# Optimization experiments

Measured on AMD Instinct MI355X. Metric: run time of the kernel, lower is better.

The kernel has to match this reference:

```python
import jax, jax.numpy as jnp
import numpy as np

D = 1024; NH = 16; HD = D // NH; B = 2; L = 2048
BASE_FAST = (1.0 + 5.0 ** 0.5) / 2.0
BASE_SLOW = 1618.0
BASE_GLU = 16180.0
ALPHA_ATTN = 0.42; ALPHA_MLP = 1.07; ALPHA_ADV = 1.0
H_GATE = max(8, D // 4)   # rope_gate hidden
H_NU = max(4, D // 8)     # DuplexViscosity hidden
LN_EPS = 1e-5


def _rope_cos_sin(seq_len, dim, base, dtype=jnp.float32):
    idx = jnp.arange(0, dim, 2, dtype=dtype) / float(dim)
    inv = 1.0 / (base ** idx)
    t = jnp.arange(seq_len, dtype=dtype)
    freqs = jnp.outer(t, inv)                       # (L, D/2)
    emb = jnp.concatenate([freqs, freqs], axis=-1)  # (L, D)
    return jnp.cos(emb)[None], jnp.sin(emb)[None]   # (1, L, D)


def _rotate_half(x):
    x1, x2 = jnp.split(x, 2, axis=-1)
    return jnp.concatenate([-x2, x1], axis=-1)


def _apply_rope(x, cos, sin):
    return x * cos + _rotate_half(x) * sin


def setup_inputs() -> dict:
    key = jax.random.key(0)
    ks = jax.random.split(key, 16)
    std = 0.02
    # all Linear weights stored as (in, out) so forward is x @ W + b
    return {
        "z": jax.random.normal(ks[0], (B, L, D), jnp.float32),
        "Wq": jax.random.normal(ks[1], (D, D), jnp.float32) * std,
        "bq": jnp.zeros((D,), jnp.float32),
        "Wk": jax.random.normal(ks[2], (D, D), jnp.float32) * std,
        "bk": jnp.zeros((D,), jnp.float32),
        "Wv": jax.random.normal(ks[3], (D, D), jnp.float32) * std,
        "bv": jnp.zeros((D,), jnp.float32),
        "Wcoh": jax.random.normal(ks[4], (D, D), jnp.float32) * std,
        "gamma": jnp.zeros((1,), jnp.float32),
        "rg_w1": jax.random.normal(ks[5], (D, H_GATE), jnp.float32) * std,
        "rg_b1": jnp.zeros((H_GATE,), jnp.float32),
        "rg_w2": jax.random.normal(ks[6], (H_GATE, 1), jnp.float32) * std,
        "rg_b2": jnp.zeros((1,), jnp.float32),
        "nu_diff": jnp.asarray(0.2, jnp.float32),
        "nu_adv": jnp.asarray(0.01, jnp.float32),
        "nu_w1": jax.random.normal(ks[7], (D, H_NU), jnp.float32) * std,
        "nu_b1": jnp.zeros((H_NU,), jnp.float32),
        "nu_w2": jax.random.normal(ks[8], (H_NU, 1), jnp.float32) * std,
        "nu_b2": jnp.zeros((1,), jnp.float32),
        "Wu": jax.random.normal(ks[9], (D, D), jnp.float32) * std,
        "bu": jnp.zeros((D,), jnp.float32),
        "Wg": jax.random.normal(ks[10], (D, D), jnp.float32) * std,
        "bg": jnp.zeros((D,), jnp.float32),
        "ln_w": jnp.ones((D,), jnp.float32),
        "ln_b": jnp.zeros((D,), jnp.float32),
        "Cw": jax.random.normal(ks[11], (D, D), jnp.float32) * std,
        "Cb": jnp.zeros((D,), jnp.float32),
    }


def reference(z, Wq, bq, Wk, bk, Wv, bv, Wcoh, gamma, rg_w1, rg_b1, rg_w2, rg_b2,
              nu_diff, nu_adv, nu_w1, nu_b1, nu_w2, nu_b2, Wu, bu, Wg, bg,
              ln_w, ln_b, Cw, Cb):
    b, l, d = z.shape
    dt = z.dtype
    # causal cumulative mean pool[t] = mean(z[0..t])
    pool = jnp.cumsum(z, axis=1) / jnp.arange(1, l + 1, dtype=dt)[None, :, None]

    # QKV projections
    Q = z @ Wq + bq
    K_raw = z @ Wk + bk
    V = z @ Wv + bv

    # global coherence bias: (B, Lq, Lk)
    gk = pool @ Wcoh
    gb = jnp.einsum('bld,bmd->blm', gk, K_raw) * (d ** -0.5)
    gb = jnp.tanh(gamma[0]) * gb

    # hybrid RoPE gate (small MLP on pool, exact gelu as in torch)
    gate = jax.nn.sigmoid(jax.nn.gelu(pool @ rg_w1 + rg_b1, approximate=False) @ rg_w2 + rg_b2)  # (B,L,1)
    cos_f, sin_f = _rope_cos_sin(l, d, BASE_FAST, dt)
    cos_s, sin_s = _rope_cos_sin(l, d, BASE_SLOW, dt)
    cos = gate * cos_f + (1.0 - gate) * cos_s
    sin = gate * sin_f + (1.0 - gate) * sin_s
    Qr = _apply_rope(Q, cos, sin)
    Kr = _apply_rope(K_raw, cos, sin)

    # multi-head causal attention with fused coherence bias
    Qh = Qr.reshape(b, l, NH, HD).transpose(0, 2, 1, 3)
    Kh = Kr.reshape(b, l, NH, HD).transpose(0, 2, 1, 3)
    Vh = V.reshape(b, l, NH, HD).transpose(0, 2, 1, 3)
    logits = jnp.einsum('bhld,bhmd->bhlm', Qh, Kh) * (HD ** -0.5)
    logits = logits + gb[:, None]
    causal = jnp.tril(jnp.ones((l, l), bool))
    logits = jnp.where(causal[None, None], logits, -jnp.inf)
    attn = jax.nn.softmax(logits, axis=-1)
    attn_out = jnp.einsum('bhlm,bhmd->bhld', attn, Vh).transpose(0, 2, 1, 3).reshape(b, l, d)
    attn_w = attn.mean(axis=1)

    # DuplexViscosity on causal pool
    delta = jnp.tanh(jnp.tanh(pool @ nu_w1 + nu_b1) @ nu_w2 + nu_b2) * jnp.abs(nu_adv)
    nu_b = jnp.abs(nu_diff) + delta  # (B,L,1)

    # GLU branch with fixed slow-base RoPE
    cos_g, sin_g = _rope_cos_sin(l, d, BASE_GLU, dt)
    z_glu = _apply_rope(z, cos_g, sin_g)
    bilinear = (z_glu @ Wu + bu) * (z_glu @ Wg + bg)
    adv = -(ALPHA_ADV * nu_b) * bilinear
    mu = adv.mean(axis=-1, keepdims=True)
    var = ((adv - mu) ** 2).mean(axis=-1, keepdims=True)
    adv_n = (adv - mu) * jax.lax.rsqrt(var + LN_EPS) * ln_w + ln_b
    mlp_out = adv_n @ Cw + Cb

    z_next = z + ALPHA_ATTN * attn_out + ALPHA_MLP * mlp_out
    return z_next, attn_w
```

## Files before the change

kernel.cpp:

```cpp
#include <hip/hip_runtime.h>

#define DD 1024
#define NHH 16
#define HDD 64
#define BB 2
#define LL 2048
#define MM (BB*LL)
#define HG 256
#define HN 128

#define LOG_FAST 0.48121182f
#define LOG_SLOW 7.3889461f
#define LOG_GLU  9.6915312f
#define SCL 0.18033688f

typedef __attribute__((ext_vector_type(8))) short short8;
typedef __attribute__((ext_vector_type(4))) float f32x4;

__device__ __forceinline__ float gelu_f(float x) {
    return 0.5f * x * (1.0f + erff(x * 0.70710678f));
}

__device__ __forceinline__ ushort f2b(float x) {
    unsigned u = __float_as_uint(x);
    unsigned r = (u + 0x7FFFu + ((u >> 16) & 1u)) >> 16;
    return (ushort)r;
}

__device__ __forceinline__ float b2f(ushort x) {
    return __uint_as_float(((unsigned)x) << 16);
}

__device__ __forceinline__ void gl_lds16(const ushort* g, ushort* l) {
    __builtin_amdgcn_global_load_lds(
        (const __attribute__((address_space(1))) unsigned int*)g,
        (__attribute__((address_space(3))) unsigned int*)l, 16, 0, 0);
}

#define SWZC(row, c8) (((((row) << 3) | ((c8) ^ ((row) & 7)))) << 3)

__device__ __forceinline__ void stage_tile(const ushort* gsrc, int rstride,
                                           ushort* lds, int tid) {
    int wid = tid >> 6;
#pragma unroll
    for (int r = 0; r < 2; ++r) {
        int c = r * 256 + tid;
        int row = c >> 3;
        int c8 = (c & 7) ^ (row & 7);
        gl_lds16(gsrc + (size_t)row * rstride + c8 * 8,
                 lds + (size_t)(r * 256 + wid * 64) * 8);
    }
}

#define LCH 128
#define NCH 16
__global__ void pool_scan1(const float* __restrict__ z, float* __restrict__ pool,
                           float* __restrict__ ctot) {
    int ch = blockIdx.x, dg = blockIdx.y, b = blockIdx.z;
    int d = dg * 256 + threadIdx.x;
    const float* zp = z + ((size_t)b * LL + ch * LCH) * DD + d;
    float* pp = pool + ((size_t)b * LL + ch * LCH) * DD + d;
    float s = 0.f;
    for (int t = 0; t < LCH; ++t) {
        s += zp[(size_t)t * DD];
        pp[(size_t)t * DD] = s;
    }
    ctot[((size_t)b * NCH + ch) * DD + d] = s;
}
__global__ void pool_scan2(const float* __restrict__ ctot, float* __restrict__ pool) {
    int ch = blockIdx.x, dg = blockIdx.y, b = blockIdx.z;
    int d = dg * 256 + threadIdx.x;
    float off = 0.f;
    for (int c = 0; c < ch; ++c) off += ctot[((size_t)b * NCH + c) * DD + d];
    int t0 = ch * LCH;
    float* pp = pool + ((size_t)b * LL + t0) * DD + d;
    for (int t = 0; t < LCH; ++t) {
        pp[(size_t)t * DD] = (pp[(size_t)t * DD] + off) / (float)(t0 + t + 1);
    }
}

__global__ void f2b_kernel(const float* __restrict__ in, ushort* __restrict__ out) {
    size_t i = ((size_t)blockIdx.x * 256 + threadIdx.x) * 4;
    float4 v = *(const float4*)&in[i];
    ushort4 o;
    o.x = f2b(v.x); o.y = f2b(v.y); o.z = f2b(v.z); o.w = f2b(v.w);
    *(ushort4*)&out[i] = o;
}

__global__ void f2bT_kernel(const float* __restrict__ W, ushort* __restrict__ Wt, int Ndim) {
    __shared__ float t[32][33];
    int n0 = blockIdx.x * 32, k0 = blockIdx.y * 32;
    int tx = threadIdx.x & 31, ty = threadIdx.x >> 5;
#pragma unroll
    for (int j = 0; j < 4; ++j)
        t[ty + j * 8][tx] = W[(size_t)(k0 + ty + j * 8) * Ndim + n0 + tx];
    __syncthreads();
#pragma unroll
    for (int j = 0; j < 4; ++j)
        Wt[(size_t)(n0 + ty + j * 8) * 1024 + k0 + tx] = f2b(t[tx][ty + j * 8]);
}

__global__ void f2bT3_kernel(const float* __restrict__ W0, const float* __restrict__ W1,
                             const float* __restrict__ W2, ushort* __restrict__ Wt) {
    const float* W = blockIdx.z == 0 ? W0 : (blockIdx.z == 1 ? W1 : W2);
    ushort* dst = Wt + (size_t)blockIdx.z * 1024 * 1024;
    __shared__ float t[32][33];
    int n0 = blockIdx.x * 32, k0 = blockIdx.y * 32;
    int tx = threadIdx.x & 31, ty = threadIdx.x >> 5;
#pragma unroll
    for (int j = 0; j < 4; ++j)
        t[ty + j * 8][tx] = W[(size_t)(k0 + ty + j * 8) * 1024 + n0 + tx];
    __syncthreads();
#pragma unroll
    for (int j = 0; j < 4; ++j)
        dst[(size_t)(n0 + ty + j * 8) * 1024 + k0 + tx] = f2b(t[tx][ty + j * 8]);
}

__global__ __launch_bounds__(256) void gemm_mfma(
        const ushort* __restrict__ A, const ushort* __restrict__ Wt,
        const float* __restrict__ bias, float* __restrict__ C, int Ndim) {
    __shared__ ushort As[4096];
    __shared__ ushort Bs[4096];
    int tid = threadIdx.x;
    int wid = tid >> 6, lane = tid & 63;
    int n0 = blockIdx.x * 128, m0 = blockIdx.y * 128;
    int wm = wid >> 1, wn = wid & 1;
    int quad = lane >> 4, l16 = lane & 15;

    f32x4 acc[4][4];
#pragma unroll
    for (int mi = 0; mi < 4; ++mi)
#pragma unroll
        for (int ni = 0; ni < 4; ++ni) acc[mi][ni] = (f32x4){0.f, 0.f, 0.f, 0.f};

    int c0 = wid * 128 + lane;
    int c1 = c0 + 64;
    const ushort* Ag0 = A + (size_t)(m0 + (c0 & 127)) * 1024 + (c0 >> 7) * 8;
    const ushort* Ag1 = A + (size_t)(m0 + (c1 & 127)) * 1024 + (c1 >> 7) * 8;
    const ushort* Bg0 = Wt + (size_t)(n0 + (c0 & 127)) * 1024 + (c0 >> 7) * 8;
    const ushort* Bg1 = Wt + (size_t)(n0 + (c1 & 127)) * 1024 + (c1 >> 7) * 8;
    ushort* Al0 = As + wid * 1024;
    ushort* Al1 = As + wid * 1024 + 512;
    ushort* Bl0 = Bs + wid * 1024;
    ushort* Bl1 = Bs + wid * 1024 + 512;

    const ushort* a_rd = &As[(quad * 128 + wm * 64 + l16) * 8];
    const ushort* b_rd = &Bs[(quad * 128 + wn * 64 + l16) * 8];

    for (int kb = 0; kb < 1024; kb += 32) {
        gl_lds16(Ag0 + kb, Al0);
        gl_lds16(Ag1 + kb, Al1);
        gl_lds16(Bg0 + kb, Bl0);
        gl_lds16(Bg1 + kb, Bl1);
        __syncthreads();
        short8 af[4], bf[4];
#pragma unroll
        for (int mi = 0; mi < 4; ++mi)
            af[mi] = *(const short8*)(a_rd + mi * 16 * 8);
#pragma unroll
        for (int ni = 0; ni < 4; ++ni)
            bf[ni] = *(const short8*)(b_rd + ni * 16 * 8);
#pragma unroll
        for (int mi = 0; mi < 4; ++mi)
#pragma unroll
            for (int ni = 0; ni < 4; ++ni)
                acc[mi][ni] = __builtin_amdgcn_mfma_f32_16x16x32_bf16(
                    af[mi], bf[ni], acc[mi][ni], 0, 0, 0);
        __syncthreads();
    }
    int bcol[4];
    float bval[4];
#pragma unroll
    for (int ni = 0; ni < 4; ++ni) {
        bcol[ni] = n0 + wn * 64 + ni * 16 + l16;
        bval[ni] = bias ? bias[bcol[ni]] : 0.f;
    }
#pragma unroll
    for (int mi = 0; mi < 4; ++mi) {
#pragma unroll
        for (int r = 0; r < 4; ++r) {
            int row = m0 + wm * 64 + mi * 16 + quad * 4 + r;
            float* Cp = C + (size_t)row * Ndim;
#pragma unroll
            for (int ni = 0; ni < 4; ++ni)
                Cp[bcol[ni]] = acc[mi][ni][r] + bval[ni];
        }
    }
}

__global__ __launch_bounds__(256) void gemm_mfma3(
        const ushort* __restrict__ A, const ushort* __restrict__ Wt,
        const float* __restrict__ b0, const float* __restrict__ b1,
        const float* __restrict__ b2, float* __restrict__ C) {
    int zid = blockIdx.z;
    const ushort* W = Wt + (size_t)zid * 1024 * 1024;
    const float* bias = zid == 0 ? b0 : (zid == 1 ? b1 : b2);
    float* Cz = C + (size_t)zid * (size_t)MM * DD;
    __shared__ ushort As[4096];
    __shared__ ushort Bs[4096];
    int tid = threadIdx.x;
    int wid = tid >> 6, lane = tid & 63;
    int n0 = blockIdx.x * 128, m0 = blockIdx.y * 128;
    int wm = wid >> 1, wn = wid & 1;
    int quad = lane >> 4, l16 = lane & 15;

    f32x4 acc[4][4];
#pragma unroll
    for (int mi = 0; mi < 4; ++mi)
#pragma unroll
        for (int ni = 0; ni < 4; ++ni) acc[mi][ni] = (f32x4){0.f, 0.f, 0.f, 0.f};

    int c0 = wid * 128 + lane;
    int c1 = c0 + 64;
    const ushort* Ag0 = A + (size_t)(m0 + (c0 & 127)) * 1024 + (c0 >> 7) * 8;
    const ushort* Ag1 = A + (size_t)(m0 + (c1 & 127)) * 1024 + (c1 >> 7) * 8;
    const ushort* Bg0 = W + (size_t)(n0 + (c0 & 127)) * 1024 + (c0 >> 7) * 8;
    const ushort* Bg1 = W + (size_t)(n0 + (c1 & 127)) * 1024 + (c1 >> 7) * 8;
    ushort* Al0 = As + wid * 1024;
    ushort* Al1 = As + wid * 1024 + 512;
    ushort* Bl0 = Bs + wid * 1024;
    ushort* Bl1 = Bs + wid * 1024 + 512;

    const ushort* a_rd = &As[(quad * 128 + wm * 64 + l16) * 8];
    const ushort* b_rd = &Bs[(quad * 128 + wn * 64 + l16) * 8];

    for (int kb = 0; kb < 1024; kb += 32) {
        gl_lds16(Ag0 + kb, Al0);
        gl_lds16(Ag1 + kb, Al1);
        gl_lds16(Bg0 + kb, Bl0);
        gl_lds16(Bg1 + kb, Bl1);
        __syncthreads();
        short8 af[4], bf[4];
#pragma unroll
        for (int mi = 0; mi < 4; ++mi)
            af[mi] = *(const short8*)(a_rd + mi * 16 * 8);
#pragma unroll
        for (int ni = 0; ni < 4; ++ni)
            bf[ni] = *(const short8*)(b_rd + ni * 16 * 8);
#pragma unroll
        for (int mi = 0; mi < 4; ++mi)
#pragma unroll
            for (int ni = 0; ni < 4; ++ni)
                acc[mi][ni] = __builtin_amdgcn_mfma_f32_16x16x32_bf16(
                    af[mi], bf[ni], acc[mi][ni], 0, 0, 0);
        __syncthreads();
    }
    float bval[4];
    int bcol[4];
#pragma unroll
    for (int ni = 0; ni < 4; ++ni) {
        bcol[ni] = n0 + wn * 64 + ni * 16 + l16;
        bval[ni] = bias[bcol[ni]];
    }
#pragma unroll
    for (int mi = 0; mi < 4; ++mi) {
#pragma unroll
        for (int r = 0; r < 4; ++r) {
            int row = m0 + wm * 64 + mi * 16 + quad * 4 + r;
            float* Cp = Cz + (size_t)row * 1024;
#pragma unroll
            for (int ni = 0; ni < 4; ++ni)
                Cp[bcol[ni]] = acc[mi][ni][r] + bval[ni];
        }
    }
}

__global__ __launch_bounds__(256) void gemm_mfma_b16out(
        const ushort* __restrict__ A, const ushort* __restrict__ Wt,
        ushort* __restrict__ C, int Ndim) {
    __shared__ ushort As[4096];
    __shared__ ushort Bs[4096];
    int tid = threadIdx.x;
    int wid = tid >> 6, lane = tid & 63;
    int n0 = blockIdx.x * 128, m0 = blockIdx.y * 128;
    int wm = wid >> 1, wn = wid & 1;
    int quad = lane >> 4, l16 = lane & 15;

    f32x4 acc[4][4];
#pragma unroll
    for (int mi = 0; mi < 4; ++mi)
#pragma unroll
        for (int ni = 0; ni < 4; ++ni) acc[mi][ni] = (f32x4){0.f, 0.f, 0.f, 0.f};

    int c0 = wid * 128 + lane;
    int c1 = c0 + 64;
    const ushort* Ag0 = A + (size_t)(m0 + (c0 & 127)) * 1024 + (c0 >> 7) * 8;
    const ushort* Ag1 = A + (size_t)(m0 + (c1 & 127)) * 1024 + (c1 >> 7) * 8;
    const ushort* Bg0 = Wt + (size_t)(n0 + (c0 & 127)) * 1024 + (c0 >> 7) * 8;
    const ushort* Bg1 = Wt + (size_t)(n0 + (c1 & 127)) * 1024 + (c1 >> 7) * 8;
    ushort* Al0 = As + wid * 1024;
    ushort* Al1 = As + wid * 1024 + 512;
    ushort* Bl0 = Bs + wid * 1024;
    ushort* Bl1 = Bs + wid * 1024 + 512;

    const ushort* a_rd = &As[(quad * 128 + wm * 64 + l16) * 8];
    const ushort* b_rd = &Bs[(quad * 128 + wn * 64 + l16) * 8];

    for (int kb = 0; kb < 1024; kb += 32) {
        gl_lds16(Ag0 + kb, Al0);
        gl_lds16(Ag1 + kb, Al1);
        gl_lds16(Bg0 + kb, Bl0);
        gl_lds16(Bg1 + kb, Bl1);
        __syncthreads();
        short8 af[4], bf[4];
#pragma unroll
        for (int mi = 0; mi < 4; ++mi)
            af[mi] = *(const short8*)(a_rd + mi * 16 * 8);
#pragma unroll
        for (int ni = 0; ni < 4; ++ni)
            bf[ni] = *(const short8*)(b_rd + ni * 16 * 8);
#pragma unroll
        for (int mi = 0; mi < 4; ++mi)
#pragma unroll
            for (int ni = 0; ni < 4; ++ni)
                acc[mi][ni] = __builtin_amdgcn_mfma_f32_16x16x32_bf16(
                    af[mi], bf[ni], acc[mi][ni], 0, 0, 0);
        __syncthreads();
    }
#pragma unroll
    for (int mi = 0; mi < 4; ++mi) {
#pragma unroll
        for (int r = 0; r < 4; ++r) {
            int row = m0 + wm * 64 + mi * 16 + quad * 4 + r;
            ushort* Cp = C + (size_t)row * Ndim;
#pragma unroll
            for (int ni = 0; ni < 4; ++ni)
                Cp[n0 + wn * 64 + ni * 16 + l16] = f2b(acc[mi][ni][r]);
        }
    }
}

__global__ __launch_bounds__(256) void gb_mfma(
        const ushort* __restrict__ gk16, const ushort* __restrict__ K16r,
        const float* __restrict__ gamma, ushort* __restrict__ gb) {
    int lt = blockIdx.x >> 4, mt = blockIdx.x & 15;
    if (mt > lt) return;
    int b = blockIdx.y;
    __shared__ ushort As[4096];
    __shared__ ushort Bs[4096];
    int tid = threadIdx.x;
    int wid = tid >> 6, lane = tid & 63;
    int l0 = lt * 128, m0 = mt * 128;
    int wm = wid >> 1, wn = wid & 1;
    int quad = lane >> 4, l16 = lane & 15;

    f32x4 acc[4][4];
#pragma unroll
    for (int mi = 0; mi < 4; ++mi)
#pragma unroll
        for (int ni = 0; ni < 4; ++ni) acc[mi][ni] = (f32x4){0.f, 0.f, 0.f, 0.f};

    int c0 = wid * 128 + lane;
    int c1 = c0 + 64;
    const ushort* Ag0 = gk16 + ((size_t)b * LL + l0 + (c0 & 127)) * 1024 + (c0 >> 7) * 8;
    const ushort* Ag1 = gk16 + ((size_t)b * LL + l0 + (c1 & 127)) * 1024 + (c1 >> 7) * 8;
    const ushort* Bg0 = K16r + ((size_t)b * LL + m0 + (c0 & 127)) * 1024 + (c0 >> 7) * 8;
    const ushort* Bg1 = K16r + ((size_t)b * LL + m0 + (c1 & 127)) * 1024 + (c1 >> 7) * 8;
    ushort* Al0 = As + wid * 1024;
    ushort* Al1 = As + wid * 1024 + 512;
    ushort* Bl0 = Bs + wid * 1024;
    ushort* Bl1 = Bs + wid * 1024 + 512;

    const ushort* a_rd = &As[(quad * 128 + wm * 64 + l16) * 8];
    const ushort* b_rd = &Bs[(quad * 128 + wn * 64 + l16) * 8];

    for (int kb = 0; kb < 1024; kb += 32) {
        gl_lds16(Ag0 + kb, Al0);
        gl_lds16(Ag1 + kb, Al1);
        gl_lds16(Bg0 + kb, Bl0);
        gl_lds16(Bg1 + kb, Bl1);
        __syncthreads();
        short8 af[4], bf[4];
#pragma unroll
        for (int mi = 0; mi < 4; ++mi)
            af[mi] = *(const short8*)(a_rd + mi * 16 * 8);
#pragma unroll
        for (int ni = 0; ni < 4; ++ni)
            bf[ni] = *(const short8*)(b_rd + ni * 16 * 8);
#pragma unroll
        for (int mi = 0; mi < 4; ++mi)
#pragma unroll
            for (int ni = 0; ni < 4; ++ni)
                acc[mi][ni] = __builtin_amdgcn_mfma_f32_16x16x32_bf16(
                    af[mi], bf[ni], acc[mi][ni], 0, 0, 0);
        __syncthreads();
    }
    float scale = tanhf(gamma[0]) * 0.25f;
#pragma unroll
    for (int mi = 0; mi < 4; ++mi) {
#pragma unroll
        for (int r = 0; r < 4; ++r) {
            int row = l0 + wm * 64 + mi * 16 + quad * 4 + r;
            ushort* Cp = gb + ((size_t)b * LL + row) * LL;
#pragma unroll
            for (int ni = 0; ni < 4; ++ni)
                Cp[m0 + wn * 64 + ni * 16 + l16] = f2b(acc[mi][ni][r] * scale);
        }
    }
}

__global__ __launch_bounds__(256) void gate_fin_kernel(
        const float* __restrict__ H1, const float* __restrict__ w2,
        const float* __restrict__ b2, float* __restrict__ gate) {
    int row = blockIdx.x, tid = threadIdx.x;
    float x = H1[(size_t)row * HG + tid];
    float val = gelu_f(x) * w2[tid];
    for (int off = 32; off; off >>= 1) val += __shfl_down(val, off);
    __shared__ float part[4];
    if ((tid & 63) == 0) part[tid >> 6] = val;
    __syncthreads();
    if (tid == 0) {
        float acc = part[0] + part[1] + part[2] + part[3] + b2[0];
        gate[row] = 1.f / (1.f + expf(-acc));
    }
}

__global__ __launch_bounds__(128) void nu_fin_kernel(
        const float* __restrict__ N1, const float* __restrict__ w2,
        const float* __restrict__ b2, const float* __restrict__ nu_diff,
        const float* __restrict__ nu_adv, float* __restrict__ nub) {
    int row = blockIdx.x, tid = threadIdx.x;
    float t = tanhf(N1[(size_t)row * HN + tid]);
    float val = t * w2[tid];
    for (int off = 32; off; off >>= 1) val += __shfl_down(val, off);
    __shared__ float part[2];
    if ((tid & 63) == 0) part[tid >> 6] = val;
    __syncthreads();
    if (tid == 0) {
        float acc = part[0] + part[1] + b2[0];
        nub[row] = fabsf(nu_diff[0]) + tanhf(acc) * fabsf(nu_adv[0]);
    }
}

__global__ void rope_qk_bf16(const float* __restrict__ Q, const float* __restrict__ K,
                             const float* __restrict__ gate,
                             ushort* __restrict__ Q16, ushort* __restrict__ K16) {
    int idx = blockIdx.x * 256 + threadIdx.x;
    int row = idx >> 9;
    int i = idx & 511;
    int b = row >> 11, t = row & (LL - 1);
    float g = gate[row];
    float fi = (float)i * (1.0f / 512.0f);
    float tf = (float)t;
    float af = tf * expf(-fi * LOG_FAST);
    float as = tf * expf(-fi * LOG_SLOW);
    float c = g * cosf(af) + (1.f - g) * cosf(as);
    float s = g * sinf(af) + (1.f - g) * sinf(as);
    size_t base = (size_t)row * DD;
    float x = Q[base + i], y = Q[base + 512 + i];
    float q1 = x * c - y * s, q2 = y * c + x * s;
    x = K[base + i]; y = K[base + 512 + i];
    float k1 = x * c - y * s, k2 = y * c + x * s;
    int h1 = i >> 6, d1 = i & 63;
    size_t o1 = ((size_t)(b * 16 + h1) * LL + t) * 64 + d1;
    size_t o2 = ((size_t)(b * 16 + 8 + h1) * LL + t) * 64 + d1;
    Q16[o1] = f2b(q1); Q16[o2] = f2b(q2);
    K16[o1] = f2b(k1); K16[o2] = f2b(k2);
}

__global__ __launch_bounds__(256) void vt16_kernel(const float* __restrict__ V,
                                                   ushort* __restrict__ VT) {
    __shared__ ushort t[64][72];
    int lb = blockIdx.x, hb = blockIdx.y, b = blockIdx.z;
    int tid = threadIdx.x;
    {
        int l = tid >> 2, c0 = (tid & 3) * 16;
        const float* Vp = V + ((size_t)(b * LL) + lb * 64 + l) * DD + hb * 64 + c0;
#pragma unroll
        for (int j = 0; j < 4; ++j) {
            float4 v = *(const float4*)(Vp + j * 4);
            t[l][c0 + j * 4 + 0] = f2b(v.x);
            t[l][c0 + j * 4 + 1] = f2b(v.y);
            t[l][c0 + j * 4 + 2] = f2b(v.z);
            t[l][c0 + j * 4 + 3] = f2b(v.w);
        }
    }
    __syncthreads();
    {
        int d = tid >> 2, l0 = (tid & 3) * 16;
        ushort tmp[16];
#pragma unroll
        for (int j = 0; j < 16; ++j) tmp[j] = t[l0 + j][d];
        ushort* Op = VT + ((size_t)((b * 16 + hb) * 64) + d) * LL + lb * 64 + l0;
        *(ushort4*)(Op + 0)  = *(ushort4*)&tmp[0];
        *(ushort4*)(Op + 4)  = *(ushort4*)&tmp[4];
        *(ushort4*)(Op + 8)  = *(ushort4*)&tmp[8];
        *(ushort4*)(Op + 12) = *(ushort4*)&tmp[12];
    }
}

__global__ void rope_glu_b16(const float* __restrict__ z, ushort* __restrict__ zg) {
    int idx = blockIdx.x * 256 + threadIdx.x;
    int row = idx >> 9;
    int i = idx & 511;
    int t = row & (LL - 1);
    float fi = (float)i * (1.0f / 512.0f);
    float ag = (float)t * expf(-fi * LOG_GLU);
    float c = cosf(ag), s = sinf(ag);
    size_t base = (size_t)row * DD;
    float x = z[base + i], y = z[base + 512 + i];
    zg[base + i]       = f2b(x * c - y * s);
    zg[base + 512 + i] = f2b(y * c + x * s);
}

__global__ __launch_bounds__(256, 3) void attn_flash_mfma(
        const ushort* __restrict__ Q16, const ushort* __restrict__ K16,
        const ushort* __restrict__ VT16, const ushort* __restrict__ gb16,
        float* __restrict__ attn_out, float* __restrict__ stats) {
    int h = blockIdx.x, qt = 31 - blockIdx.y, b = blockIdx.z;
    __shared__ ushort Qs[4096], Ks[2][4096], Vs[2][4096];
    __shared__ ushort Ps[4][1152];
    int tid = threadIdx.x, wid = tid >> 6, lane = tid & 63;
    int quad = lane >> 4, l16 = lane & 15;
    const ushort* Qg = Q16 + ((size_t)(b * 16 + h) * LL) * 64;
    const ushort* Kg = K16 + ((size_t)(b * 16 + h) * LL) * 64;
    const ushort* Vg = VT16 + ((size_t)(b * 16 + h) * 64) * LL;
    const ushort* gbB = gb16 + (size_t)b * LL * LL;
    float* stB = stats + ((size_t)(b * 16 + h) * LL) * 2;
    int qrow = wid * 16 + quad * 4;
    int q0 = qt * 64;

    stage_tile(Qg + (size_t)q0 * 64, 64, Qs, tid);
    stage_tile(Kg, 64, Ks[0], tid);
    stage_tile(Vg, LL, Vs[0], tid);
    __syncthreads();
    short8 qf[2];
#pragma unroll
    for (int ks = 0; ks < 2; ++ks)
        qf[ks] = *(const short8*)(Qs + SWZC(wid * 16 + l16, ks * 4 + quad));

    short ov = (l16 == 0) ? (short)0x3F80 : (short)0;
    short8 onesf = {ov, ov, ov, ov, ov, ov, ov, ov};

    f32x4 ofr[5];
    float m_r[4];
#pragma unroll
    for (int nt = 0; nt < 5; ++nt) ofr[nt] = (f32x4){0.f, 0.f, 0.f, 0.f};
#pragma unroll
    for (int r = 0; r < 4; ++r) m_r[r] = -3e38f;

    for (int kt = 0; kt <= qt; ++kt) {
        int cur = kt & 1;
        int k0 = kt * 64;
        ushort gw[4][4];
#pragma unroll
        for (int r = 0; r < 4; ++r) {
            const ushort* gp = gbB + (size_t)(q0 + qrow + r) * LL + k0 + l16;
#pragma unroll
            for (int nt = 0; nt < 4; ++nt) gw[nt][r] = gp[nt * 16];
        }
        if (kt < qt) {
            stage_tile(Kg + (size_t)(k0 + 64) * 64, 64, Ks[cur ^ 1], tid);
            stage_tile(Vg + (k0 + 64), LL, Vs[cur ^ 1], tid);
        }
        f32x4 sf[4];
#pragma unroll
        for (int nt = 0; nt < 4; ++nt)
#pragma unroll
            for (int r = 0; r < 4; ++r) sf[nt][r] = b2f(gw[nt][r]);
#pragma unroll
        for (int ks = 0; ks < 2; ++ks)
#pragma unroll
            for (int nt = 0; nt < 4; ++nt) {
                short8 kf = *(const short8*)(Ks[cur] + SWZC(nt * 16 + l16, ks * 4 + quad));
                sf[nt] = __builtin_amdgcn_mfma_f32_16x16x32_bf16(qf[ks], kf, sf[nt], 0, 0, 0);
            }
        if (kt == qt) {
#pragma unroll
            for (int nt = 0; nt < 4; ++nt)
#pragma unroll
                for (int r = 0; r < 4; ++r)
                    if (nt * 16 + l16 > qrow + r) sf[nt][r] = -1e30f;
        }
        float alpha[4], mS[4];
#pragma unroll
        for (int r = 0; r < 4; ++r) {
            float m = fmaxf(fmaxf(sf[0][r], sf[1][r]), fmaxf(sf[2][r], sf[3][r]));
#pragma unroll
            for (int off = 1; off < 16; off <<= 1)
                m = fmaxf(m, __shfl_xor(m, off));
            float nm = fmaxf(m_r[r], m);
            alpha[r] = __builtin_amdgcn_exp2f((m_r[r] - nm) * SCL);
            m_r[r] = nm;
            mS[r] = nm * SCL;
        }
#pragma unroll
        for (int nt = 0; nt < 4; ++nt)
#pragma unroll
            for (int r = 0; r < 4; ++r) {
                float p = __builtin_amdgcn_exp2f(fmaf(sf[nt][r], SCL, -mS[r]));
                Ps[wid][(quad * 4 + r) * 72 + nt * 16 + l16] = f2b(p);
            }
#pragma unroll
        for (int nt = 0; nt < 5; ++nt)
#pragma unroll
            for (int r = 0; r < 4; ++r) ofr[nt][r] *= alpha[r];
        short8 pf[2];
#pragma unroll
        for (int ks = 0; ks < 2; ++ks)
            pf[ks] = *(const short8*)(Ps[wid] + l16 * 72 + ks * 32 + quad * 8);
#pragma unroll
        for (int ks = 0; ks < 2; ++ks) {
#pragma unroll
            for (int nt = 0; nt < 4; ++nt) {
                short8 vf = *(const short8*)(Vs[cur] + SWZC(nt * 16 + l16, ks * 4 + quad));
                ofr[nt] = __builtin_amdgcn_mfma_f32_16x16x32_bf16(pf[ks], vf, ofr[nt], 0, 0, 0);
            }
            ofr[4] = __builtin_amdgcn_mfma_f32_16x16x32_bf16(pf[ks], onesf, ofr[4], 0, 0, 0);
        }
        __syncthreads();
    }
#pragma unroll
    for (int r = 0; r < 4; ++r) {
        float l = __shfl(ofr[4][r], (lane & 48));
        float rinv = 1.0f / l;
        float* op = attn_out + ((size_t)(b * LL) + q0 + qrow + r) * DD + h * 64 + l16;
#pragma unroll
        for (int nt = 0; nt < 4; ++nt)
            op[nt * 16] = ofr[nt][r] * rinv;
    }
    if (l16 == 0) {
#pragma unroll
        for (int r = 0; r < 4; ++r) {
            size_t si = (size_t)(q0 + qrow + r) * 2;
            stB[si]     = m_r[r];
            stB[si + 1] = ofr[4][r];
        }
    }
}

__global__ __launch_bounds__(256, 4) void attn_w_mfma(
        const ushort* __restrict__ Q16, const ushort* __restrict__ K16,
        const ushort* __restrict__ gb16, const float* __restrict__ stats,
        float* __restrict__ aw) {
    int qt = blockIdx.x >> 5, kt = blockIdx.x & 31;
    int b = blockIdx.y;
    int tid = threadIdx.x, wid = tid >> 6, lane = tid & 63;
    int quad = lane >> 4, l16 = lane & 15;
    int q0 = qt * 64, k0 = kt * 64;
    int qrow = wid * 16 + quad * 4;
    if (kt > qt) {
        int rr = tid >> 2, c0 = (tid & 3) * 16;
        float4 zv = make_float4(0.f, 0.f, 0.f, 0.f);
        float* p = aw + ((size_t)(b * LL) + q0 + rr) * LL + k0 + c0;
#pragma unroll
        for (int j = 0; j < 4; ++j) *(float4*)(p + j * 4) = zv;
        return;
    }
    __shared__ ushort Qs[2][4096], Ks[2][4096];
    float acc[4][4];
#pragma unroll
    for (int nt = 0; nt < 4; ++nt)
#pragma unroll
        for (int r = 0; r < 4; ++r) acc[nt][r] = 0.f;
    f32x4 gacc[4];
    const ushort* gbB = gb16 + (size_t)b * LL * LL;
#pragma unroll
    for (int r = 0; r < 4; ++r) {
        const ushort* gp = gbB + (size_t)(q0 + qrow + r) * LL + k0 + l16;
#pragma unroll
        for (int nt = 0; nt < 4; ++nt) gacc[nt][r] = b2f(gp[nt * 16]);
    }
    bool diag = (kt == qt);
    stage_tile(Q16 + ((size_t)(b * 16) * LL + q0) * 64, 64, Qs[0], tid);
    stage_tile(K16 + ((size_t)(b * 16) * LL + k0) * 64, 64, Ks[0], tid);
    __syncthreads();
    for (int h = 0; h < NHH; ++h) {
        int cur = h & 1;
        float mS[4], li[4];
        const float* sp = stats + ((size_t)(b * 16 + h) * LL + q0 + qrow) * 2;
#pragma unroll
        for (int r = 0; r < 4; ++r) {
            mS[r] = sp[r * 2] * SCL;
            li[r] = 1.0f / sp[r * 2 + 1];
        }
        if (h < 15) {
            stage_tile(Q16 + ((size_t)(b * 16 + h + 1) * LL + q0) * 64, 64, Qs[cur ^ 1], tid);
            stage_tile(K16 + ((size_t)(b * 16 + h + 1) * LL + k0) * 64, 64, Ks[cur ^ 1], tid);
        }
        short8 qf[2];
#pragma unroll
        for (int ks = 0; ks < 2; ++ks)
            qf[ks] = *(const short8*)(Qs[cur] + SWZC(wid * 16 + l16, ks * 4 + quad));
        f32x4 sf[4];
#pragma unroll
        for (int nt = 0; nt < 4; ++nt) sf[nt] = gacc[nt];
#pragma unroll
        for (int ks = 0; ks < 2; ++ks)
#pragma unroll
            for (int nt = 0; nt < 4; ++nt) {
                short8 kf = *(const short8*)(Ks[cur] + SWZC(nt * 16 + l16, ks * 4 + quad));
                sf[nt] = __builtin_amdgcn_mfma_f32_16x16x32_bf16(qf[ks], kf, sf[nt], 0, 0, 0);
            }
#pragma unroll
        for (int nt = 0; nt < 4; ++nt)
#pragma unroll
            for (int r = 0; r < 4; ++r) {
                int row = qrow + r;
                if (!diag || (nt * 16 + l16 <= row))
                    acc[nt][r] += __builtin_amdgcn_exp2f(fmaf(sf[nt][r], SCL, -mS[r])) * li[r];
            }
        __syncthreads();
    }
#pragma unroll
    for (int r = 0; r < 4; ++r) {
        float* op = aw + ((size_t)(b * LL) + q0 + qrow + r) * LL + k0 + l16;
#pragma unroll
        for (int nt = 0; nt < 4; ++nt)
            op[nt * 16] = acc[nt][r] * 0.0625f;
    }
}

__global__ __launch_bounds__(256) void adv_ln_kernel(
        const float* __restrict__ U, const float* __restrict__ G,
        const float* __restrict__ nub, const float* __restrict__ lnw,
        const float* __restrict__ lnb, ushort* __restrict__ out) {
    int row = blockIdx.x, tid = threadIdx.x;
    size_t base = (size_t)row * DD + tid * 4;
    float4 u4 = *(const float4*)&U[base];
    float4 g4 = *(const float4*)&G[base];
    float nu = nub[row];
    float a[4];
    a[0] = -nu * u4.x * g4.x;
    a[1] = -nu * u4.y * g4.y;
    a[2] = -nu * u4.z * g4.z;
    a[3] = -nu * u4.w * g4.w;
    float ts = a[0] + a[1] + a[2] + a[3];
    float tq = a[0] * a[0] + a[1] * a[1] + a[2] * a[2] + a[3] * a[3];
    for (int off = 32; off; off >>= 1) {
        ts += __shfl_down(ts, off);
        tq += __shfl_down(tq, off);
    }
    __shared__ float r1[4], r2[4];
    if ((tid & 63) == 0) { r1[tid >> 6] = ts; r2[tid >> 6] = tq; }
    __syncthreads();
    __shared__ float s_mu, s_rs;
    if (tid == 0) {
        float S  = r1[0] + r1[1] + r1[2] + r1[3];
        float Qq = r2[0] + r2[1] + r2[2] + r2[3];
        float mu = S * (1.0f / 1024.f);
        float var = Qq * (1.0f / 1024.f) - mu * mu;
        s_mu = mu;
        s_rs = rsqrtf(var + 1e-5f);
    }
    __syncthreads();
    float mu = s_mu, rs = s_rs;
    float4 w4 = *(const float4*)&lnw[tid * 4];
    float4 b4 = *(const float4*)&lnb[tid * 4];
    ushort4 ov;
    ov.x = f2b((a[0] - mu) * rs * w4.x + b4.x);
    ov.y = f2b((a[1] - mu) * rs * w4.y + b4.y);
    ov.z = f2b((a[2] - mu) * rs * w4.z + b4.z);
    ov.w = f2b((a[3] - mu) * rs * w4.w + b4.w);
    *(ushort4*)&out[base] = ov;
}

__global__ void final_kernel(const float* __restrict__ z, const float* __restrict__ ao,
                             const float* __restrict__ mlp, float* __restrict__ out) {
    size_t i = ((size_t)blockIdx.x * 256 + threadIdx.x) * 4;
    float4 z4 = *(const float4*)&z[i];
    float4 a4 = *(const float4*)&ao[i];
    float4 m4 = *(const float4*)&mlp[i];
    float4 o;
    o.x = z4.x + 0.42f * a4.x + 1.07f * m4.x;
    o.y = z4.y + 0.42f * a4.y + 1.07f * m4.y;
    o.z = z4.z + 0.42f * a4.z + 1.07f * m4.z;
    o.w = z4.w + 0.42f * a4.w + 1.07f * m4.w;
    *(float4*)&out[i] = o;
}

extern "C" void kernel_launch(void* const* d_in, const int* in_sizes, int n_in,
                              void* d_out, int out_size, void* d_ws, size_t ws_size,
                              hipStream_t stream) {
    const float* z       = (const float*)d_in[0];
    const float* Wq      = (const float*)d_in[1];
    const float* bq      = (const float*)d_in[2];
    const float* Wk      = (const float*)d_in[3];
    const float* bk      = (const float*)d_in[4];
    const float* Wv      = (const float*)d_in[5];
    const float* bv      = (const float*)d_in[6];
    const float* Wcoh    = (const float*)d_in[7];
    const float* gamma   = (const float*)d_in[8];
    const float* rg_w1   = (const float*)d_in[9];
    const float* rg_b1   = (const float*)d_in[10];
    const float* rg_w2   = (const float*)d_in[11];
    const float* rg_b2   = (const float*)d_in[12];
    const float* nu_diff = (const float*)d_in[13];
    const float* nu_adv  = (const float*)d_in[14];
    const float* nu_w1   = (const float*)d_in[15];
    const float* nu_b1   = (const float*)d_in[16];
    const float* nu_w2   = (const float*)d_in[17];
    const float* nu_b2   = (const float*)d_in[18];
    const float* Wu      = (const float*)d_in[19];
    const float* bu      = (const float*)d_in[20];
    const float* Wg      = (const float*)d_in[21];
    const float* bg      = (const float*)d_in[22];
    const float* ln_w    = (const float*)d_in[23];
    const float* ln_b    = (const float*)d_in[24];
    const float* Cw      = (const float*)d_in[25];
    const float* Cb      = (const float*)d_in[26];

    float* out_z  = (float*)d_out;
    float* out_aw = out_z + (size_t)MM * DD;

    float* ws = (float*)d_ws;
    const size_t MD = (size_t)MM * DD;
    float* pool  = ws;
    float* Qb    = ws + MD;
    float* Kb    = ws + 2 * MD;
    float* Vb    = ws + 3 * MD;
    float* gkb   = ws + 4 * MD;
    float* gbb   = ws + 5 * MD;
    float* H1    = ws + 7 * MD;
    float* N1    = H1 + (size_t)MM * HG;
    float* gate  = N1 + (size_t)MM * HN;
    float* nub   = gate + MM;
    float* stats = nub + MM;
    float* ctot  = stats + (size_t)BB * NHH * LL * 2;

    char* gbase  = (char*)gbb;
    ushort* Ab   = (ushort*)gbase;
    ushort* Wb   = (ushort*)(gbase + (size_t)8 * 1024 * 1024);
    ushort* gb16 = (ushort*)(gbase + (size_t)16 * 1024 * 1024);
    ushort* Q16  = (ushort*)Vb;
    ushort* K16  = (ushort*)Vb + MD;
    ushort* VT16 = (ushort*)pool;
    ushort* gk16 = (ushort*)gkb;
    ushort* K16r = (ushort*)gkb + MD;

    dim3 g128(8, 32);
    dim3 cvt_g(4096);
    dim3 wT_g(32, 32);

    pool_scan1<<<dim3(NCH, 4, BB), 256, 0, stream>>>(z, pool, ctot);
    pool_scan2<<<dim3(NCH, 4, BB), 256, 0, stream>>>(ctot, pool);
    f2b_kernel<<<cvt_g, 256, 0, stream>>>(z, Ab);
    f2bT3_kernel<<<dim3(32, 32, 3), 256, 0, stream>>>(Wq, Wk, Wv, Wb);
    gemm_mfma3<<<dim3(8, 32, 3), 256, 0, stream>>>(Ab, Wb, bq, bk, bv, Qb);
    f2b_kernel<<<cvt_g, 256, 0, stream>>>(Kb, K16r);
    f2b_kernel<<<cvt_g, 256, 0, stream>>>(pool, Ab);
    f2bT_kernel<<<wT_g, 256, 0, stream>>>(Wcoh, Wb, DD);
    gemm_mfma_b16out<<<g128, 256, 0, stream>>>(Ab, Wb, gk16, DD);
    f2bT_kernel<<<dim3(8, 32), 256, 0, stream>>>(rg_w1, Wb, HG);
    gemm_mfma<<<dim3(2, 32), 256, 0, stream>>>(Ab, Wb, rg_b1, H1, HG);
    f2bT_kernel<<<dim3(4, 32), 256, 0, stream>>>(nu_w1, Wb, HN);
    gemm_mfma<<<dim3(1, 32), 256, 0, stream>>>(Ab, Wb, nu_b1, N1, HN);
    gb_mfma<<<dim3(256, BB), 256, 0, stream>>>(gk16, K16r, gamma, gb16);
    gate_fin_kernel<<<dim3(MM), 256, 0, stream>>>(H1, rg_w2, rg_b2, gate);
    nu_fin_kernel<<<dim3(MM), 128, 0, stream>>>(N1, nu_w2, nu_b2, nu_diff, nu_adv, nub);
    vt16_kernel<<<dim3(32, 16, BB), 256, 0, stream>>>(Vb, VT16);
    rope_qk_bf16<<<dim3((MM * 512) / 256), 256, 0, stream>>>(Qb, Kb, gate, Q16, K16);
    attn_flash_mfma<<<dim3(NHH, 32, BB), 256, 0, stream>>>(Q16, K16, VT16, gb16, gkb, stats);
    attn_w_mfma<<<dim3(1024, BB), 256, 0, stream>>>(Q16, K16, gb16, stats, out_aw);
    rope_glu_b16<<<dim3((MM * 512) / 256), 256, 0, stream>>>(z, Ab);
    f2bT3_kernel<<<dim3(32, 32, 2), 256, 0, stream>>>(Wu, Wg, Wg, Wb);
    gemm_mfma3<<<dim3(8, 32, 2), 256, 0, stream>>>(Ab, Wb, bu, bg, bg, Qb);
    adv_ln_kernel<<<dim3(MM), 256, 0, stream>>>(Qb, Kb, nub, ln_w, ln_b, Ab);
    f2bT_kernel<<<wT_g, 256, 0, stream>>>(Cw, Wb, DD);
    gemm_mfma<<<g128, 256, 0, stream>>>(Ab, Wb, Cb, Qb, DD);
    final_kernel<<<dim3(MD / 4 / 256), 256, 0, stream>>>(z, gkb, Qb, out_z);
}
```

Measured before the change: 626.5 us.

## Fuse conversions into scans/GEMMs, merge gate kernels, shrink flash-attention LDS

Folds the bf16 conversions of z, pool and K into the pool scans and the QKV GEMM epilogue, removing three standalone conversion passes. Weight transposes are batched into fewer launches, and the rope-gate and viscosity first-layer GEMMs and their finishing kernels are each merged into one kernel. The flash-attention kernel reuses the Q buffer for P, single-buffers V and raises its occupancy hint from 3 to 4 blocks per SM, which frees LDS but exposes the V load to less overlap. Overall the change cuts launches and global memory traffic, at the cost of more workspace aliasing that has to stay correct.

```diff
diff --git a/kernel.cpp b/kernel.cpp
--- a/kernel.cpp
+++ b/kernel.cpp
@@ -54,50 +54,73 @@
 
 #define LCH 128
 #define NCH 16
-__global__ void pool_scan1(const float* __restrict__ z, float* __restrict__ pool,
-                           float* __restrict__ ctot) {
+__global__ void pool_scan1(const float* __restrict__ z, float* __restrict__ part,
+                           float* __restrict__ ctot, ushort* __restrict__ zb) {
     int ch = blockIdx.x, dg = blockIdx.y, b = blockIdx.z;
     int d = dg * 256 + threadIdx.x;
-    const float* zp = z + ((size_t)b * LL + ch * LCH) * DD + d;
-    float* pp = pool + ((size_t)b * LL + ch * LCH) * DD + d;
+    size_t base = ((size_t)b * LL + ch * LCH) * DD + d;
+    const float* zp = z + base;
+    float* pp = part + base;
+    ushort* zo = zb + base;
     float s = 0.f;
     for (int t = 0; t < LCH; ++t) {
-        s += zp[(size_t)t * DD];
+        float v = zp[(size_t)t * DD];
+        s += v;
         pp[(size_t)t * DD] = s;
+        zo[(size_t)t * DD] = f2b(v);
     }
     ctot[((size_t)b * NCH + ch) * DD + d] = s;
 }
-__global__ void pool_scan2(const float* __restrict__ ctot, float* __restrict__ pool) {
+__global__ void pool_scan2(const float* __restrict__ part, const float* __restrict__ ctot,
+                           ushort* __restrict__ poolb) {
     int ch = blockIdx.x, dg = blockIdx.y, b = blockIdx.z;
     int d = dg * 256 + threadIdx.x;
     float off = 0.f;
     for (int c = 0; c < ch; ++c) off += ctot[((size_t)b * NCH + c) * DD + d];
     int t0 = ch * LCH;
-    float* pp = pool + ((size_t)b * LL + t0) * DD + d;
+    size_t base = ((size_t)b * LL + t0) * DD + d;
+    const float* pp = part + base;
+    ushort* po = poolb + base;
     for (int t = 0; t < LCH; ++t) {
-        pp[(size_t)t * DD] = (pp[(size_t)t * DD] + off) / (float)(t0 + t + 1);
-    }
-}
-
-__global__ void f2b_kernel(const float* __restrict__ in, ushort* __restrict__ out) {
-    size_t i = ((size_t)blockIdx.x * 256 + threadIdx.x) * 4;
-    float4 v = *(const float4*)&in[i];
-    ushort4 o;
-    o.x = f2b(v.x); o.y = f2b(v.y); o.z = f2b(v.z); o.w = f2b(v.w);
-    *(ushort4*)&out[i] = o;
-}
-
-__global__ void f2bT_kernel(const float* __restrict__ W, ushort* __restrict__ Wt, int Ndim) {
+        po[(size_t)t * DD] = f2b((pp[(size_t)t * DD] + off) / (float)(t0 + t + 1));
+    }
+}
+
+__global__ void f2bT4_kernel(const float* __restrict__ W0, const float* __restrict__ W1,
+                             const float* __restrict__ W2, const float* __restrict__ W3,
+                             ushort* __restrict__ Wt) {
+    const float* W = blockIdx.z == 0 ? W0 : (blockIdx.z == 1 ? W1 :
+                     (blockIdx.z == 2 ? W2 : W3));
+    ushort* dst = Wt + (size_t)blockIdx.z * 1024 * 1024;
     __shared__ float t[32][33];
     int n0 = blockIdx.x * 32, k0 = blockIdx.y * 32;
     int tx = threadIdx.x & 31, ty = threadIdx.x >> 5;
 #pragma unroll
     for (int j = 0; j < 4; ++j)
+        t[ty + j * 8][tx] = W[(size_t)(k0 + ty + j * 8) * 1024 + n0 + tx];
+    __syncthreads();
+#pragma unroll
+    for (int j = 0; j < 4; ++j)
+        dst[(size_t)(n0 + ty + j * 8) * 1024 + k0 + tx] = f2b(t[tx][ty + j * 8]);
+}
+
+__global__ void f2bT_rgnu(const float* __restrict__ Wrg, const float* __restrict__ Wnu,
+                          ushort* __restrict__ WtRG, ushort* __restrict__ WtNU) {
+    int zc = blockIdx.z;
+    if (zc == 1 && blockIdx.x >= 4) return;
+    const float* W = zc == 0 ? Wrg : Wnu;
+    ushort* dst = zc == 0 ? WtRG : WtNU;
+    int Ndim = zc == 0 ? HG : HN;
+    __shared__ float t[32][33];
+    int n0 = blockIdx.x * 32, k0 = blockIdx.y * 32;
+    int tx = threadIdx.x & 31, ty = threadIdx.x >> 5;
+#pragma unroll
+    for (int j = 0; j < 4; ++j)
         t[ty + j * 8][tx] = W[(size_t)(k0 + ty + j * 8) * Ndim + n0 + tx];
     __syncthreads();
 #pragma unroll
     for (int j = 0; j < 4; ++j)
-        Wt[(size_t)(n0 + ty + j * 8) * 1024 + k0 + tx] = f2b(t[tx][ty + j * 8]);
+        dst[(size_t)(n0 + ty + j * 8) * 1024 + k0 + tx] = f2b(t[tx][ty + j * 8]);
 }
 
 __global__ void f2bT3_kernel(const float* __restrict__ W0, const float* __restrict__ W1,
@@ -191,7 +214,8 @@
 __global__ __launch_bounds__(256) void gemm_mfma3(
         const ushort* __restrict__ A, const ushort* __restrict__ Wt,
         const float* __restrict__ b0, const float* __restrict__ b1,
-        const float* __restrict__ b2, float* __restrict__ C) {
+        const float* __restrict__ b2, float* __restrict__ C,
+        ushort* __restrict__ K16r) {
     int zid = blockIdx.z;
     const ushort* W = Wt + (size_t)zid * 1024 * 1024;
     const float* bias = zid == 0 ? b0 : (zid == 1 ? b1 : b2);
@@ -252,15 +276,20 @@
         bcol[ni] = n0 + wn * 64 + ni * 16 + l16;
         bval[ni] = bias[bcol[ni]];
     }
+    bool doK = (zid == 1) && (K16r != nullptr);
 #pragma unroll
     for (int mi = 0; mi < 4; ++mi) {
 #pragma unroll
         for (int r = 0; r < 4; ++r) {
             int row = m0 + wm * 64 + mi * 16 + quad * 4 + r;
             float* Cp = Cz + (size_t)row * 1024;
-#pragma unroll
-            for (int ni = 0; ni < 4; ++ni)
-                Cp[bcol[ni]] = acc[mi][ni][r] + bval[ni];
+            ushort* Kp = K16r + (size_t)row * 1024;
+#pragma unroll
+            for (int ni = 0; ni < 4; ++ni) {
+                float v = acc[mi][ni][r] + bval[ni];
+                Cp[bcol[ni]] = v;
+                if (doK) Kp[bcol[ni]] = f2b(v);
+            }
         }
     }
 }
@@ -326,6 +355,87 @@
 #pragma unroll
             for (int ni = 0; ni < 4; ++ni)
                 Cp[n0 + wn * 64 + ni * 16 + l16] = f2b(acc[mi][ni][r]);
+        }
+    }
+}
+
+__global__ __launch_bounds__(256) void gemm_gates(
+        const ushort* __restrict__ A, const ushort* __restrict__ WtRG,
+        const ushort* __restrict__ WtNU, const float* __restrict__ rg_b1,
+        const float* __restrict__ nu_b1, float* __restrict__ H1,
+        float* __restrict__ N1) {
+    int bx = blockIdx.x;
+    bool isH = bx < 2;
+    const ushort* Wt = isH ? WtRG : WtNU;
+    const float* bias = isH ? rg_b1 : nu_b1;
+    float* C = isH ? H1 : N1;
+    int Ndim = isH ? HG : HN;
+    int n0 = isH ? bx * 128 : 0;
+    int m0 = blockIdx.y * 128;
+    __shared__ ushort As[4096];
+    __shared__ ushort Bs[4096];
+    int tid = threadIdx.x;
+    int wid = tid >> 6, lane = tid & 63;
+    int wm = wid >> 1, wn = wid & 1;
+    int quad = lane >> 4, l16 = lane & 15;
+
+    f32x4 acc[4][4];
+#pragma unroll
+    for (int mi = 0; mi < 4; ++mi)
+#pragma unroll
+        for (int ni = 0; ni < 4; ++ni) acc[mi][ni] = (f32x4){0.f, 0.f, 0.f, 0.f};
+
+    int c0 = wid * 128 + lane;
+    int c1 = c0 + 64;
+    const ushort* Ag0 = A + (size_t)(m0 + (c0 & 127)) * 1024 + (c0 >> 7) * 8;
+    const ushort* Ag1 = A + (size_t)(m0 + (c1 & 127)) * 1024 + (c1 >> 7) * 8;
+    const ushort* Bg0 = Wt + (size_t)(n0 + (c0 & 127)) * 1024 + (c0 >> 7) * 8;
+    const ushort* Bg1 = Wt + (size_t)(n0 + (c1 & 127)) * 1024 + (c1 >> 7) * 8;
+    ushort* Al0 = As + wid * 1024;
+    ushort* Al1 = As + wid * 1024 + 512;
+    ushort* Bl0 = Bs + wid * 1024;
+    ushort* Bl1 = Bs + wid * 1024 + 512;
+
+    const ushort* a_rd = &As[(quad * 128 + wm * 64 + l16) * 8];
+    const ushort* b_rd = &Bs[(quad * 128 + wn * 64 + l16) * 8];
+
+    for (int kb = 0; kb < 1024; kb += 32) {
+        gl_lds16(Ag0 + kb, Al0);
+        gl_lds16(Ag1 + kb, Al1);
+        gl_lds16(Bg0 + kb, Bl0);
+        gl_lds16(Bg1 + kb, Bl1);
+        __syncthreads();
+        short8 af[4], bf[4];
+#pragma unroll
+        for (int mi = 0; mi < 4; ++mi)
+            af[mi] = *(const short8*)(a_rd + mi * 16 * 8);
+#pragma unroll
+        for (int ni = 0; ni < 4; ++ni)
+            bf[ni] = *(const short8*)(b_rd + ni * 16 * 8);
+#pragma unroll
+        for (int mi = 0; mi < 4; ++mi)
+#pragma unroll
+            for (int ni = 0; ni < 4; ++ni)
+                acc[mi][ni] = __builtin_amdgcn_mfma_f32_16x16x32_bf16(
+                    af[mi], bf[ni], acc[mi][ni], 0, 0, 0);
+        __syncthreads();
+    }
+    int bcol[4];
+    float bval[4];
+#pragma unroll
+    for (int ni = 0; ni < 4; ++ni) {
+        bcol[ni] = n0 + wn * 64 + ni * 16 + l16;
+        bval[ni] = bias[bcol[ni]];
+    }
+#pragma unroll
+    for (int mi = 0; mi < 4; ++mi) {
+#pragma unroll
+        for (int r = 0; r < 4; ++r) {
+            int row = m0 + wm * 64 + mi * 16 + quad * 4 + r;
+            float* Cp = C + (size_t)row * Ndim;
+#pragma unroll
+            for (int ni = 0; ni < 4; ++ni)
+                Cp[bcol[ni]] = acc[mi][ni][r] + bval[ni];
         }
     }
 }
@@ -399,36 +509,27 @@
     }
 }
 
-__global__ __launch_bounds__(256) void gate_fin_kernel(
-        const float* __restrict__ H1, const float* __restrict__ w2,
-        const float* __restrict__ b2, float* __restrict__ gate) {
+__global__ __launch_bounds__(256) void gatenu_fin(
+        const float* __restrict__ H1, const float* __restrict__ N1,
+        const float* __restrict__ rg_w2, const float* __restrict__ rg_b2,
+        const float* __restrict__ nu_w2, const float* __restrict__ nu_b2,
+        const float* __restrict__ nu_diff, const float* __restrict__ nu_adv,
+        float* __restrict__ gate, float* __restrict__ nub) {
     int row = blockIdx.x, tid = threadIdx.x;
-    float x = H1[(size_t)row * HG + tid];
-    float val = gelu_f(x) * w2[tid];
-    for (int off = 32; off; off >>= 1) val += __shfl_down(val, off);
-    __shared__ float part[4];
-    if ((tid & 63) == 0) part[tid >> 6] = val;
+    float gv = gelu_f(H1[(size_t)row * HG + tid]) * rg_w2[tid];
+    float nv = (tid < HN) ? tanhf(N1[(size_t)row * HN + tid]) * nu_w2[tid] : 0.f;
+    for (int off = 32; off; off >>= 1) {
+        gv += __shfl_down(gv, off);
+        nv += __shfl_down(nv, off);
+    }
+    __shared__ float pg[4], pn[4];
+    if ((tid & 63) == 0) { pg[tid >> 6] = gv; pn[tid >> 6] = nv; }
     __syncthreads();
     if (tid == 0) {
-        float acc = part[0] + part[1] + part[2] + part[3] + b2[0];
-        gate[row] = 1.f / (1.f + expf(-acc));
-    }
-}
-
-__global__ __launch_bounds__(128) void nu_fin_kernel(
-        const float* __restrict__ N1, const float* __restrict__ w2,
-        const float* __restrict__ b2, const float* __restrict__ nu_diff,
-        const float* __restrict__ nu_adv, float* __restrict__ nub) {
-    int row = blockIdx.x, tid = threadIdx.x;
-    float t = tanhf(N1[(size_t)row * HN + tid]);
-    float val = t * w2[tid];
-    for (int off = 32; off; off >>= 1) val += __shfl_down(val, off);
-    __shared__ float part[2];
-    if ((tid & 63) == 0) part[tid >> 6] = val;
-    __syncthreads();
-    if (tid == 0) {
-        float acc = part[0] + part[1] + b2[0];
-        nub[row] = fabsf(nu_diff[0]) + tanhf(acc) * fabsf(nu_adv[0]);
+        float ga = pg[0] + pg[1] + pg[2] + pg[3] + rg_b2[0];
+        gate[row] = 1.f / (1.f + expf(-ga));
+        float na = pn[0] + pn[1] + pn[2] + pn[3] + nu_b2[0];
+        nub[row] = fabsf(nu_diff[0]) + tanhf(na) * fabsf(nu_adv[0]);
     }
 }
 
@@ -503,13 +604,14 @@
     zg[base + 512 + i] = f2b(y * c + x * s);
 }
 
-__global__ __launch_bounds__(256, 3) void attn_flash_mfma(
+__global__ __launch_bounds__(256, 4) void attn_flash_mfma(
         const ushort* __restrict__ Q16, const ushort* __restrict__ K16,
         const ushort* __restrict__ VT16, const ushort* __restrict__ gb16,
         float* __restrict__ attn_out, float* __restrict__ stats) {
     int h = blockIdx.x, qt = 31 - blockIdx.y, b = blockIdx.z;
-    __shared__ ushort Qs[4096], Ks[2][4096], Vs[2][4096];
-    __shared__ ushort Ps[4][1152];
+    __shared__ ushort QP[4608];
+    __shared__ ushort Ks[2][4096];
+    __shared__ ushort Vs[4096];
     int tid = threadIdx.x, wid = tid >> 6, lane = tid & 63;
     int quad = lane >> 4, l16 = lane & 15;
     const ushort* Qg = Q16 + ((size_t)(b * 16 + h) * LL) * 64;
@@ -520,14 +622,16 @@
     int qrow = wid * 16 + quad * 4;
     int q0 = qt * 64;
 
-    stage_tile(Qg + (size_t)q0 * 64, 64, Qs, tid);
+    stage_tile(Qg + (size_t)q0 * 64, 64, QP, tid);
     stage_tile(Kg, 64, Ks[0], tid);
-    stage_tile(Vg, LL, Vs[0], tid);
+    stage_tile(Vg, LL, Vs, tid);
     __syncthreads();
     short8 qf[2];
 #pragma unroll
     for (int ks = 0; ks < 2; ++ks)
-        qf[ks] = *(const short8*)(Qs + SWZC(wid * 16 + l16, ks * 4 + quad));
+        qf[ks] = *(const short8*)(QP + SWZC(wid * 16 + l16, ks * 4 + quad));
+    __syncthreads();
+    ushort* Pw = QP + wid * 1152;
 
     short ov = (l16 == 0) ? (short)0x3F80 : (short)0;
     short8 onesf = {ov, ov, ov, ov, ov, ov, ov, ov};
@@ -549,10 +653,9 @@
 #pragma unroll
             for (int nt = 0; nt < 4; ++nt) gw[nt][r] = gp[nt * 16];
         }
-        if (kt < qt) {
-            stage_tile(Kg + (size_t)(k0 + 64) * 64, 64, Ks[cur ^ 1], tid);
-            stage_tile(Vg + (k0 + 64), LL, Vs[cur ^ 1], tid);
-        }
+        if (kt > 0) stage_tile(Vg + k0, LL, Vs, tid);
+        if (kt < qt) stage_tile(Kg + (size_t)(k0 + 64) * 64, 64, Ks[cur ^ 1], tid);
+
         f32x4 sf[4];
 #pragma unroll
         for (int nt = 0; nt < 4; ++nt)
@@ -589,7 +692,7 @@
 #pragma unroll
             for (int r = 0; r < 4; ++r) {
                 float p = __builtin_amdgcn_exp2f(fmaf(sf[nt][r], SCL, -mS[r]));
-                Ps[wid][(quad * 4 + r) * 72 + nt * 16 + l16] = f2b(p);
+                Pw[(quad * 4 + r) * 72 + nt * 16 + l16] = f2b(p);
             }
 #pragma unroll
         for (int nt = 0; nt < 5; ++nt)
@@ -598,12 +701,12 @@
         short8 pf[2];
 #pragma unroll
         for (int ks = 0; ks < 2; ++ks)
-            pf[ks] = *(const short8*)(Ps[wid] + l16 * 72 + ks * 32 + quad * 8);
+            pf[ks] = *(const short8*)(Pw + l16 * 72 + ks * 32 + quad * 8);
 #pragma unroll
         for (int ks = 0; ks < 2; ++ks) {
 #pragma unroll
             for (int nt = 0; nt < 4; ++nt) {
-                short8 vf = *(const short8*)(Vs[cur] + SWZC(nt * 16 + l16, ks * 4 + quad));
+                short8 vf = *(const short8*)(Vs + SWZC(nt * 16 + l16, ks * 4 + quad));
                 ofr[nt] = __builtin_amdgcn_mfma_f32_16x16x32_bf16(pf[ks], vf, ofr[nt], 0, 0, 0);
             }
             ofr[4] = __builtin_amdgcn_mfma_f32_16x16x32_bf16(pf[ks], onesf, ofr[4], 0, 0, 0);
@@ -822,41 +925,37 @@
     ushort* Ab   = (ushort*)gbase;
     ushort* Wb   = (ushort*)(gbase + (size_t)8 * 1024 * 1024);
     ushort* gb16 = (ushort*)(gbase + (size_t)16 * 1024 * 1024);
+    ushort* WtRG = Wb;
+    ushort* WtNU = Wb + (size_t)1024 * 1024;
     ushort* Q16  = (ushort*)Vb;
     ushort* K16  = (ushort*)Vb + MD;
     ushort* VT16 = (ushort*)pool;
+    ushort* poolb = (ushort*)pool;
+    float*  part = gkb;
     ushort* gk16 = (ushort*)gkb;
     ushort* K16r = (ushort*)gkb + MD;
 
     dim3 g128(8, 32);
-    dim3 cvt_g(4096);
     dim3 wT_g(32, 32);
 
-    pool_scan1<<<dim3(NCH, 4, BB), 256, 0, stream>>>(z, pool, ctot);
-    pool_scan2<<<dim3(NCH, 4, BB), 256, 0, stream>>>(ctot, pool);
-    f2b_kernel<<<cvt_g, 256, 0, stream>>>(z, Ab);
-    f2bT3_kernel<<<dim3(32, 32, 3), 256, 0, stream>>>(Wq, Wk, Wv, Wb);
-    gemm_mfma3<<<dim3(8, 32, 3), 256, 0, stream>>>(Ab, Wb, bq, bk, bv, Qb);
-    f2b_kernel<<<cvt_g, 256, 0, stream>>>(Kb, K16r);
-    f2b_kernel<<<cvt_g, 256, 0, stream>>>(pool, Ab);
-    f2bT_kernel<<<wT_g, 256, 0, stream>>>(Wcoh, Wb, DD);
-    gemm_mfma_b16out<<<g128, 256, 0, stream>>>(Ab, Wb, gk16, DD);
-    f2bT_kernel<<<dim3(8, 32), 256, 0, stream>>>(rg_w1, Wb, HG);
-    gemm_mfma<<<dim3(2, 32), 256, 0, stream>>>(Ab, Wb, rg_b1, H1, HG);
-    f2bT_kernel<<<dim3(4, 32), 256, 0, stream>>>(nu_w1, Wb, HN);
-    gemm_mfma<<<dim3(1, 32), 256, 0, stream>>>(Ab, Wb, nu_b1, N1, HN);
+    pool_scan1<<<dim3(NCH, 4, BB), 256, 0, stream>>>(z, part, ctot, Ab);
+    pool_scan2<<<dim3(NCH, 4, BB), 256, 0, stream>>>(part, ctot, poolb);
+    f2bT4_kernel<<<dim3(32, 32, 4), 256, 0, stream>>>(Wq, Wk, Wv, Wcoh, Wb);
+    gemm_mfma3<<<dim3(8, 32, 3), 256, 0, stream>>>(Ab, Wb, bq, bk, bv, Qb, K16r);
+    gemm_mfma_b16out<<<g128, 256, 0, stream>>>(poolb, Wb + (size_t)3 * 1024 * 1024, gk16, DD);
+    f2bT_rgnu<<<dim3(8, 32, 2), 256, 0, stream>>>(rg_w1, nu_w1, WtRG, WtNU);
+    gemm_gates<<<dim3(3, 32), 256, 0, stream>>>(poolb, WtRG, WtNU, rg_b1, nu_b1, H1, N1);
     gb_mfma<<<dim3(256, BB), 256, 0, stream>>>(gk16, K16r, gamma, gb16);
-    gate_fin_kernel<<<dim3(MM), 256, 0, stream>>>(H1, rg_w2, rg_b2, gate);
-    nu_fin_kernel<<<dim3(MM), 128, 0, stream>>>(N1, nu_w2, nu_b2, nu_diff, nu_adv, nub);
+    gatenu_fin<<<dim3(MM), 256, 0, stream>>>(H1, N1, rg_w2, rg_b2, nu_w2, nu_b2,
+                                             nu_diff, nu_adv, gate, nub);
     vt16_kernel<<<dim3(32, 16, BB), 256, 0, stream>>>(Vb, VT16);
     rope_qk_bf16<<<dim3((MM * 512) / 256), 256, 0, stream>>>(Qb, Kb, gate, Q16, K16);
     attn_flash_mfma<<<dim3(NHH, 32, BB), 256, 0, stream>>>(Q16, K16, VT16, gb16, gkb, stats);
     attn_w_mfma<<<dim3(1024, BB), 256, 0, stream>>>(Q16, K16, gb16, stats, out_aw);
     rope_glu_b16<<<dim3((MM * 512) / 256), 256, 0, stream>>>(z, Ab);
-    f2bT3_kernel<<<dim3(32, 32, 2), 256, 0, stream>>>(Wu, Wg, Wg, Wb);
-    gemm_mfma3<<<dim3(8, 32, 2), 256, 0, stream>>>(Ab, Wb, bu, bg, bg, Qb);
+    f2bT3_kernel<<<dim3(32, 32, 3), 256, 0, stream>>>(Wu, Wg, Cw, Wb);
+    gemm_mfma3<<<dim3(8, 32, 2), 256, 0, stream>>>(Ab, Wb, bu, bg, bg, Qb, nullptr);
     adv_ln_kernel<<<dim3(MM), 256, 0, stream>>>(Qb, Kb, nub, ln_w, ln_b, Ab);
-    f2bT_kernel<<<wT_g, 256, 0, stream>>>(Cw, Wb, DD);
-    gemm_mfma<<<g128, 256, 0, stream>>>(Ab, Wb, Cb, Qb, DD);
+    gemm_mfma<<<g128, 256, 0, stream>>>(Ab, Wb + (size_t)2 * 1024 * 1024, Cb, Qb, DD);
     final_kernel<<<dim3(MD / 4 / 256), 256, 0, stream>>>(z, gkb, Qb, out_z);
 }
```

After: 582.7 us. 1.08x faster.
